# Optimization experiments

Measured on AMD Instinct MI355X. Metric: run time of the kernel, lower is better.

## Reference

```python
import jax, jax.numpy as jnp
import numpy as np

H, HKV, D, W = 64, 8, 64, 128          # heads, kv heads, head_dim, sliding window
G = H // HKV                            # query heads per kv head
HID = 2880
THETA = 150000.0
SCALE = D ** -0.5
NEG = -1e30


def _rope(x, positions):
    # x: [B,S,h,D]; GPT-NeoX style rotate_half RoPE
    half = D // 2
    inv_freq = 1.0 / (THETA ** (jnp.arange(0, half, dtype=jnp.float32) / half))
    ang = positions.astype(jnp.float32)[:, None] * inv_freq          # [S, D/2]
    cos = jnp.cos(ang)[None, :, None, :]
    sin = jnp.sin(ang)[None, :, None, :]
    x1, x2 = x[..., :half], x[..., half:]
    return jnp.concatenate([x1 * cos - x2 * sin, x2 * cos + x1 * sin], axis=-1)


def setup_inputs() -> dict:
    key = jax.random.key(0)
    ks = jax.random.split(key, 6)
    B, S = 1, 2048
    return {
        "hidden_states": jax.random.normal(ks[0], (B, S, HID), jnp.float32),
        "positions": jnp.arange(S, dtype=jnp.int32),
        "w_qkv": jax.random.normal(ks[1], (HID, (H + 2 * HKV) * D), jnp.float32) * 0.02,
        "b_qkv": jax.random.normal(ks[2], ((H + 2 * HKV) * D,), jnp.float32) * 0.02,
        "w_o": jax.random.normal(ks[3], (H * D, HID), jnp.float32) * 0.02,
        "b_o": jax.random.normal(ks[4], (HID,), jnp.float32) * 0.02,
        "sinks": jax.random.normal(ks[5], (H,), jnp.float32),
    }


def reference(hidden_states, positions, w_qkv, b_qkv, w_o, b_o, sinks):
    B, S, _ = hidden_states.shape
    qkv = hidden_states @ w_qkv + b_qkv                               # [B,S,(H+2Hkv)*D]
    q, k, v = jnp.split(qkv, [H * D, H * D + HKV * D], axis=-1)
    Q = q.reshape(B, S, H, D)
    K = k.reshape(B, S, HKV, D)
    V = v.reshape(B, S, HKV, D)
    Q = _rope(Q, positions)
    K = _rope(K, positions)

    # banded (sliding-window) key/value gather: query i sees keys i-W+1..i
    offsets = jnp.arange(W) - (W - 1)                                 # [-(W-1)..0]
    kidx = jnp.arange(S)[:, None] + offsets                           # [S,W]
    valid = kidx >= 0
    kidx = jnp.maximum(kidx, 0)
    Kw = K[:, kidx]                                                    # [B,S,W,HKV,D]
    Vw = V[:, kidx]

    Qr = Q.reshape(B, S, HKV, G, D)                                    # GQA grouping
    scores = jnp.einsum('bskgd,bswkd->bskgw', Qr, Kw) * SCALE          # [B,S,HKV,G,W]
    scores = jnp.where(valid[None, :, None, None, :], scores, NEG)

    sink = sinks.reshape(HKV, G)[None, None]                           # [1,1,HKV,G]
    m = jnp.maximum(scores.max(axis=-1), sink)                         # [B,S,HKV,G]
    p = jnp.exp(scores - m[..., None])
    denom = p.sum(axis=-1) + jnp.exp(sink - m)                         # sink in normalizer
    out = jnp.einsum('bskgw,bswkd->bskgd', p, Vw) / denom[..., None]

    out = out.reshape(B, S, H * D)
    return out @ w_o + b_o
```

## Files before the change

kernel.cpp:

```cpp
#include <hip/hip_runtime.h>

typedef unsigned short u16;
typedef __bf16 bf16x8 __attribute__((ext_vector_type(8)));
typedef float f32x4 __attribute__((ext_vector_type(4)));
typedef unsigned short u16x8 __attribute__((ext_vector_type(8)));

#define QKV_N 5120
#define SEQ 2048
#define ATTN_K 4096
#define KPAD 2944
#define SCALE 0.125f
#define NEGINF -1e30f

__device__ __forceinline__ u16 f2bf(float f) {
  unsigned int u = __builtin_bit_cast(unsigned int, f);
  u = (u + 0x7FFFu + ((u >> 16) & 1u)) >> 16;
  return (u16)u;
}
__device__ __forceinline__ float bf2f(u16 u) {
  unsigned int x = ((unsigned int)u) << 16;
  return __builtin_bit_cast(float, x);
}

#define MFMA16(a, b, c) __builtin_amdgcn_mfma_f32_16x16x32_bf16((a), (b), (c), 0, 0, 0)

__device__ __forceinline__ void gl_lds16(const u16* g, u16* l) {
  __builtin_amdgcn_global_load_lds(
      (const __attribute__((address_space(1))) unsigned int*)(const void*)g,
      (__attribute__((address_space(3))) unsigned int*)(void*)l, 16, 0, 0);
}

__device__ __forceinline__ bf16x8 fragrd(const u16* base, int row, int rb) {
  return *(const bf16x8*)((const char*)(base + row * 32) + rb);
}

__device__ __forceinline__ bf16x8 lds_frag(const u16* mat, int row, int kh, int lg) {
  int off = row * 128 + ((kh * 64 + lg * 16) ^ ((row & 7) << 4));
  return *(const bf16x8*)((const char*)mat + off);
}

__global__ __launch_bounds__(256) void k_rope_table(const int* __restrict__ pos,
                                                    float2* __restrict__ tab) {
  int t = blockIdx.x * 256 + threadIdx.x;
  int s = t >> 5, i = t & 31;
  float freq = powf(150000.0f, -(float)i * (1.0f / 32.0f));
  float ang = (float)pos[s] * freq;
  float sv, cv;
  sincosf(ang, &sv, &cv);
  tab[t] = make_float2(cv, sv);
}

__global__ __launch_bounds__(256) void k_convert_pad(const float* __restrict__ in,
                                                     u16* __restrict__ out) {
  int i = blockIdx.x * 256 + threadIdx.x;
  int r = i / 736, c4 = i - r * 736;
  if (r >= 2048) return;
  ushort4 o = {0, 0, 0, 0};
  if (c4 < 720) {
    float4 v = *(const float4*)(in + (size_t)r * 2880 + c4 * 4);
    o.x = f2bf(v.x); o.y = f2bf(v.y); o.z = f2bf(v.z); o.w = f2bf(v.w);
  }
  ((ushort4*)out)[(size_t)r * 736 + c4] = o;
}

__global__ __launch_bounds__(256) void k_transpose(const float* __restrict__ in,
                                                   u16* __restrict__ out,
                                                   int Kin, int Kout, int Nd, int Npad) {
  __shared__ float tile[32][33];
  int n0 = blockIdx.x * 32, k0 = blockIdx.y * 32;
  int c = threadIdx.x & 31, r0 = threadIdx.x >> 5;
#pragma unroll
  for (int j = 0; j < 4; j++) {
    int r = r0 + j * 8;
    float v = 0.f;
    if (n0 + c < Nd && k0 + r < Kin) v = in[(size_t)(k0 + r) * Nd + n0 + c];
    tile[r][c] = v;
  }
  __syncthreads();
#pragma unroll
  for (int j = 0; j < 4; j++) {
    int rr = r0 + j * 8;
    int n = n0 + rr;
    if (n < Npad) out[(size_t)n * Kout + k0 + c] = f2bf(tile[c][rr]);
  }
}

__global__ __launch_bounds__(256, 2) void k_gemm1(const u16* __restrict__ Ag,
                                                  const u16* __restrict__ Bg,
                                                  const float* __restrict__ bias,
                                                  u16* __restrict__ C) {
  __shared__ u16 lds_[2][18432];
  u16* L = &lds_[0][0];
  const int tid = threadIdx.x;
  const int lane = tid & 63, wave = tid >> 6;
  const int wm = wave >> 1, wn = wave & 1;
  const int lr = lane & 15, lg = lane >> 4;
  const int bid = blockIdx.x;
  const int xcd = bid & 7, j = bid >> 3;
  const int m0 = (j >> 2) * 128;
  const int n0 = (xcd * 4 + (j & 3)) * 160;

  f32x4 acc[4][5] = {};
  bf16x8 Bf[5], Af0, Af1;

  const int rb = (lg * 16) ^ (((lr >> 1) & 3) << 4);
  const int arow = tid >> 2;
  const int axs = ((tid & 3) ^ ((tid >> 3) & 3)) << 3;

  size_t boff[5];
#pragma unroll
  for (int r_ = 0; r_ < 5; r_++) {
    int e = r_ * 2048 + tid * 8;
    int bkh = (e >= 5120) ? 1 : 0;
    int re = e - bkh * 5120;
    int brow = re >> 5;
    int bch = (re >> 3) & 3;
    int bps = bch ^ ((brow >> 1) & 3);
    boff[r_] = (size_t)(n0 + brow) * KPAD + bkh * 32 + bps * 8;
  }

#define STA(b, kh, kt, r_)                                                      \
  gl_lds16(Ag + (size_t)(m0 + (r_) * 64 + arow) * KPAD + (kt) + (kh) * 32 + axs, \
           L + (b) * 18432 + (kh) * 4096 + (r_) * 2048 + wave * 512)
#define STB(b, kt, r_)                                                          \
  gl_lds16(Bg + boff[r_] + (kt), L + (b) * 18432 + 8192 + (r_) * 2048 + wave * 512)
#define RDB(b, kh)                                                              \
  { _Pragma("unroll") for (int nf = 0; nf < 5; nf++)                            \
      Bf[nf] = fragrd(L + (b) * 18432 + 8192 + (kh) * 5120,                     \
                      wn * 80 + nf * 16 + lr, rb); }
#define RDA(b, kh, mf0_)                                                        \
  { Af0 = fragrd(L + (b) * 18432 + (kh) * 4096, wm * 64 + (mf0_) * 16 + lr, rb); \
    Af1 = fragrd(L + (b) * 18432 + (kh) * 4096, wm * 64 + ((mf0_) + 1) * 16 + lr, rb); }
#define MM(ma, mb)                                                              \
  { __builtin_amdgcn_s_setprio(1);                                              \
    _Pragma("unroll") for (int nf = 0; nf < 5; nf++) {                          \
      acc[ma][nf] = MFMA16(Af0, Bf[nf], acc[ma][nf]);                           \
      acc[mb][nf] = MFMA16(Af1, Bf[nf], acc[mb][nf]); }                         \
    __builtin_amdgcn_s_setprio(0); }
#define BAR __builtin_amdgcn_s_barrier();
#define VM4 asm volatile("s_waitcnt vmcnt(4)" ::: "memory");
#define VM0 asm volatile("s_waitcnt vmcnt(0)" ::: "memory");

  STA(0, 0, 0, 0); STA(0, 0, 0, 1);
  STB(0, 0, 0); STB(0, 0, 1); STB(0, 0, 2); STB(0, 0, 3); STB(0, 0, 4);
  STA(0, 1, 0, 0); STA(0, 1, 0, 1);
  VM4 BAR

  for (int t = 0; t < 46; t++) {
    const int b = t & 1, nb = b ^ 1;
    const int kt1 = (t + 1) * 64;
    const bool st = (t < 45);
    RDB(b, 0) RDA(b, 0, 0)
    if (st) { STA(nb, 0, kt1, 0); STA(nb, 0, kt1, 1); STB(nb, kt1, 0); }
    BAR MM(0, 1) BAR
    RDA(b, 0, 2)
    if (st) { STB(nb, kt1, 1); STB(nb, kt1, 2); VM4 } else { VM0 }
    BAR MM(2, 3) BAR
    RDB(b, 1) RDA(b, 1, 0)
    if (st) { STB(nb, kt1, 3); STB(nb, kt1, 4); }
    BAR MM(0, 1) BAR
    RDA(b, 1, 2)
    if (st) { STA(nb, 1, kt1, 0); STA(nb, 1, kt1, 1); VM4 }
    BAR MM(2, 3) BAR
  }
#undef STA
#undef STB
#undef RDB
#undef RDA
#undef MM
#undef BAR
#undef VM4
#undef VM0

#pragma unroll
  for (int mf = 0; mf < 4; mf++)
#pragma unroll
    for (int nf = 0; nf < 5; nf++) {
      int col = n0 + wn * 80 + nf * 16 + lr;
      float bv = bias[col];
#pragma unroll
      for (int rg = 0; rg < 4; rg++) {
        int row = m0 + wm * 64 + mf * 16 + lg * 4 + rg;
        C[(size_t)row * QKV_N + col] = f2bf(acc[mf][nf][rg] + bv);
      }
    }
}

__global__ __launch_bounds__(256, 2) void k_gemm2(const u16* __restrict__ Ag,
                                                  const u16* __restrict__ Bg,
                                                  const float* __restrict__ bias,
                                                  float* __restrict__ C) {
  __shared__ u16 ldsbuf[2][16384];
  const int tid = threadIdx.x;
  const int lane = tid & 63, wave = tid >> 6;
  const int wm = wave >> 1, wn = wave & 1;
  const int lr = lane & 15, lg = lane >> 4;
  int bid = blockIdx.x;
  int l = (bid & 7) * 46 + (bid >> 3);
  const int m0 = (l & 15) * 128, n0 = (l >> 4) * 128;

  f32x4 acc[4][4] = {};

  const int srow = wave * 8 + (lane >> 3);
  const int sc = ((lane & 7) ^ (lane >> 3)) << 3;
  const u16* gA = Ag + (size_t)(m0 + srow) * ATTN_K + sc;
  const u16* gB = Bg + (size_t)(n0 + srow) * ATTN_K + sc;

#define G2_STAGE(kt, b)                                                          \
  {                                                                              \
    u16* Ab = &ldsbuf[b][0];                                                     \
    u16* Bb = &ldsbuf[b][8192];                                                  \
    _Pragma("unroll") for (int r = 0; r < 4; r++) {                              \
      gl_lds16(gA + (size_t)(r * 32) * ATTN_K + (kt), Ab + (r * 32 + wave * 8) * 64); \
      gl_lds16(gB + (size_t)(r * 32) * ATTN_K + (kt), Bb + (r * 32 + wave * 8) * 64); \
    }                                                                            \
  }

  G2_STAGE(0, 0)
  G2_STAGE(64, 1)
  asm volatile("s_waitcnt vmcnt(8)" ::: "memory");
  __builtin_amdgcn_s_barrier();

  for (int t = 0; t < 64; t++) {
    const int b = t & 1;
    const u16* La = &ldsbuf[b][0];
    const u16* Lb = &ldsbuf[b][8192];
    bf16x8 Bf[4][2];
#pragma unroll
    for (int nf = 0; nf < 4; nf++)
#pragma unroll
      for (int kh = 0; kh < 2; kh++)
        Bf[nf][kh] = lds_frag(Lb, wn * 64 + nf * 16 + lr, kh, lg);
    bf16x8 Af[2][2];
#pragma unroll
    for (int mi = 0; mi < 2; mi++)
#pragma unroll
      for (int kh = 0; kh < 2; kh++)
        Af[mi][kh] = lds_frag(La, wm * 64 + mi * 16 + lr, kh, lg);
#pragma unroll
    for (int q = 0; q < 2; q++) {
      bf16x8 An[2][2];
      if (q < 1) {
#pragma unroll
        for (int mi = 0; mi < 2; mi++)
#pragma unroll
          for (int kh = 0; kh < 2; kh++)
            An[mi][kh] = lds_frag(La, wm * 64 + ((q + 1) * 2 + mi) * 16 + lr, kh, lg);
      }
      __builtin_amdgcn_s_setprio(1);
#pragma unroll
      for (int mi = 0; mi < 2; mi++)
#pragma unroll
        for (int nf = 0; nf < 4; nf++)
#pragma unroll
          for (int kh = 0; kh < 2; kh++)
            acc[q * 2 + mi][nf] = MFMA16(Af[mi][kh], Bf[nf][kh], acc[q * 2 + mi][nf]);
      __builtin_amdgcn_s_setprio(0);
      if (q < 1) {
#pragma unroll
        for (int mi = 0; mi < 2; mi++)
#pragma unroll
          for (int kh = 0; kh < 2; kh++)
            Af[mi][kh] = An[mi][kh];
      }
    }
    __builtin_amdgcn_s_barrier();
    if (t <= 61) {
      G2_STAGE((t + 2) * 64, b)
      asm volatile("s_waitcnt vmcnt(8)" ::: "memory");
    } else {
      asm volatile("s_waitcnt vmcnt(0)" ::: "memory");
    }
    __builtin_amdgcn_s_barrier();
  }
#undef G2_STAGE

#pragma unroll
  for (int mi = 0; mi < 4; mi++)
#pragma unroll
    for (int ni = 0; ni < 4; ni++) {
      int row = m0 + wm * 64 + mi * 16 + lg * 4;
      int col = n0 + wn * 64 + ni * 16 + lr;
      if (col < 2880) {
        float bv = bias[col];
#pragma unroll
        for (int rg = 0; rg < 4; rg++)
          C[(size_t)(row + rg) * 2880 + col] = acc[mi][ni][rg] + bv;
      }
    }
}

__global__ __launch_bounds__(512, 2) void k_attn(const u16* __restrict__ qkv,
                                                 const float* __restrict__ sinks,
                                                 const float2* __restrict__ tab,
                                                 u16* __restrict__ out) {
  __shared__ u16 Klds[160 * 64];
  __shared__ u16 Vt[64 * 168];
  __shared__ u16 Pslab[8 * 32 * 40];
  const int hk = blockIdx.y;
  const int s0 = blockIdx.x * 32;
  const int kb = s0 - 127;
  const int tid = threadIdx.x;
  const int lane = tid & 63, w = tid >> 6;
  const int lr = lane & 15, lg = lane >> 4;

  for (int u = tid; u < 160 * 4; u += 512) {
    int key = u >> 2, c = u & 3;
    int kidx = kb + key;
    u16x8 v1 = {0, 0, 0, 0, 0, 0, 0, 0}, v2 = v1;
    if (kidx >= 0 && kidx < SEQ) {
      const u16* base = qkv + (size_t)kidx * QKV_N + 4096 + hk * 64;
      u16x8 x1 = *(const u16x8*)(base + c * 8);
      u16x8 x2 = *(const u16x8*)(base + 32 + c * 8);
      const float2* cs = tab + (size_t)kidx * 32 + c * 8;
#pragma unroll
      for (int j = 0; j < 8; j++) {
        float f1 = bf2f(x1[j]), f2 = bf2f(x2[j]);
        float2 t = cs[j];
        v1[j] = f2bf(f1 * t.x - f2 * t.y);
        v2[j] = f2bf(f2 * t.x + f1 * t.y);
      }
    }
    int o1 = (key * 128 + c * 16) ^ ((key & 7) << 4);
    int o2 = (key * 128 + (c + 4) * 16) ^ ((key & 7) << 4);
    *(u16x8*)((char*)Klds + o1) = v1;
    *(u16x8*)((char*)Klds + o2) = v2;
  }
  for (int e4 = tid; e4 < 160 * 16; e4 += 512) {
    int key = e4 >> 4, d0 = (e4 & 15) * 4;
    int kidx = kb + key;
    ushort4 v = {0, 0, 0, 0};
    if (kidx >= 0 && kidx < SEQ)
      v = *(const ushort4*)(qkv + (size_t)kidx * QKV_N + 4608 + hk * 64 + d0);
    Vt[(d0 + 0) * 168 + key] = v.x;
    Vt[(d0 + 1) * 168 + key] = v.y;
    Vt[(d0 + 2) * 168 + key] = v.z;
    Vt[(d0 + 3) * 168 + key] = v.w;
  }

  const int head = hk * 8 + w;
  bf16x8 qf[2][2];
#pragma unroll
  for (int rt = 0; rt < 2; rt++) {
    int s = s0 + rt * 16 + lr;
    const u16* base = qkv + (size_t)s * QKV_N + head * 64 + lg * 8;
    u16x8 r0 = *(const u16x8*)(base);
    u16x8 r1 = *(const u16x8*)(base + 32);
    const float2* cs = tab + (size_t)s * 32 + lg * 8;
    u16x8 y0, y1;
#pragma unroll
    for (int j = 0; j < 8; j++) {
      float f1 = bf2f(r0[j]), f2 = bf2f(r1[j]);
      float2 t = cs[j];
      y0[j] = f2bf(f1 * t.x - f2 * t.y);
      y1[j] = f2bf(f2 * t.x + f1 * t.y);
    }
    qf[rt][0] = __builtin_bit_cast(bf16x8, y0);
    qf[rt][1] = __builtin_bit_cast(bf16x8, y1);
  }
  __syncthreads();

  f32x4 sc[2][10];
  f32x4 zz = {0.f, 0.f, 0.f, 0.f};
#pragma unroll
  for (int rt = 0; rt < 2; rt++)
#pragma unroll
    for (int nt = 0; nt < 10; nt++) sc[rt][nt] = zz;
#pragma unroll
  for (int nt = 0; nt < 10; nt++) {
    int key = nt * 16 + lr;
#pragma unroll
    for (int ks = 0; ks < 2; ks++) {
      int off = (key * 128 + ks * 64 + lg * 16) ^ ((key & 7) << 4);
      bf16x8 kf = *(const bf16x8*)((const char*)Klds + off);
      sc[0][nt] = MFMA16(qf[0][ks], kf, sc[0][nt]);
      sc[1][nt] = MFMA16(qf[1][ks], kf, sc[1][nt]);
    }
  }

#pragma unroll
  for (int rt = 0; rt < 2; rt++)
#pragma unroll
    for (int nt = 0; nt < 10; nt++)
#pragma unroll
      for (int rg = 0; rg < 4; rg++) {
        int qq = rt * 16 + lg * 4 + rg;
        int j = nt * 16 + lr;
        bool valid = (j >= qq) && (j <= qq + 127) && ((kb + j) >= 0);
        sc[rt][nt][rg] = valid ? sc[rt][nt][rg] * SCALE : NEGINF;
      }

  const float sink = sinks[head];
  float den[2][4];
#pragma unroll
  for (int rt = 0; rt < 2; rt++)
#pragma unroll
    for (int rg = 0; rg < 4; rg++) {
      float m = NEGINF;
#pragma unroll
      for (int nt = 0; nt < 10; nt++) m = fmaxf(m, sc[rt][nt][rg]);
#pragma unroll
      for (int x = 1; x < 16; x <<= 1) m = fmaxf(m, __shfl_xor(m, x, 64));
      m = fmaxf(m, sink);
      float sum = 0.f;
#pragma unroll
      for (int nt = 0; nt < 10; nt++) {
        float p = __expf(sc[rt][nt][rg] - m);
        sc[rt][nt][rg] = p;
        sum += p;
      }
#pragma unroll
      for (int x = 1; x < 16; x <<= 1) sum += __shfl_xor(sum, x, 64);
      den[rt][rg] = sum + __expf(sink - m);
    }

  f32x4 oacc[2][4];
#pragma unroll
  for (int rt = 0; rt < 2; rt++)
#pragma unroll
    for (int dn = 0; dn < 4; dn++) oacc[rt][dn] = zz;
  u16* slab = &Pslab[w * 32 * 40];
#pragma unroll
  for (int kt = 0; kt < 5; kt++) {
#pragma unroll
    for (int rt = 0; rt < 2; rt++)
#pragma unroll
      for (int j2 = 0; j2 < 2; j2++)
#pragma unroll
        for (int rg = 0; rg < 4; rg++)
          slab[(rt * 16 + lg * 4 + rg) * 40 + j2 * 16 + lr] = f2bf(sc[rt][kt * 2 + j2][rg]);
    asm volatile("s_waitcnt lgkmcnt(0)" ::: "memory");
    __builtin_amdgcn_sched_barrier(0);
    bf16x8 pf0 = *(const bf16x8*)&slab[lr * 40 + lg * 8];
    bf16x8 pf1 = *(const bf16x8*)&slab[(16 + lr) * 40 + lg * 8];
#pragma unroll
    for (int dn = 0; dn < 4; dn++) {
      bf16x8 vf = *(const bf16x8*)&Vt[(dn * 16 + lr) * 168 + kt * 32 + lg * 8];
      oacc[0][dn] = MFMA16(pf0, vf, oacc[0][dn]);
      oacc[1][dn] = MFMA16(pf1, vf, oacc[1][dn]);
    }
  }

#pragma unroll
  for (int rt = 0; rt < 2; rt++)
#pragma unroll
    for (int dn = 0; dn < 4; dn++)
#pragma unroll
      for (int rg = 0; rg < 4; rg++) {
        int s = s0 + rt * 16 + lg * 4 + rg;
        float val = oacc[rt][dn][rg] / den[rt][rg];
        out[(size_t)s * ATTN_K + head * 64 + dn * 16 + lr] = f2bf(val);
      }
}

extern "C" void kernel_launch(void* const* d_in, const int* in_sizes, int n_in,
                              void* d_out, int out_size, void* d_ws, size_t ws_size,
                              hipStream_t stream) {
  const float* hs = (const float*)d_in[0];
  const int* pos = (const int*)d_in[1];
  const float* wqkv = (const float*)d_in[2];
  const float* bqkv = (const float*)d_in[3];
  const float* wo = (const float*)d_in[4];
  const float* bo = (const float*)d_in[5];
  const float* sinks = (const float*)d_in[6];
  float* out = (float*)d_out;

  char* ws = (char*)d_ws;
  u16* qkvb = (u16*)(ws + 0);
  u16* hsb = (u16*)(ws + 41943040);
  u16* wqkvT = (u16*)(ws + 54001664);
  u16* attnb = (u16*)(ws + 41943040);
  u16* woT = (u16*)(ws + 84148224);
  float2* tab = (float2*)(ws + 108265472);

  k_rope_table<<<256, 256, 0, stream>>>(pos, tab);
  k_convert_pad<<<5888, 256, 0, stream>>>(hs, hsb);
  k_transpose<<<dim3(160, 92), 256, 0, stream>>>(wqkv, wqkvT, 2880, KPAD, 5120, 5120);
  k_transpose<<<dim3(92, 128), 256, 0, stream>>>(wo, woT, 4096, 4096, 2880, 2944);
  k_gemm1<<<512, 256, 0, stream>>>(hsb, wqkvT, bqkv, qkvb);
  k_attn<<<dim3(64, 8), 512, 0, stream>>>(qkvb, sinks, tab, attnb);
  k_gemm2<<<368, 256, 0, stream>>>(attnb, woT, bo, out);
}
```

Before: 199.1 us.

## Merge gemm1 A-fragment phases and retile gemm2 to 128x96 tiles

In the QKV GEMM, all four A fragments are now loaded at once, so each k-half runs one block of 20 MFMAs instead of two blocks of 10. This halves the barrier pairs per iteration, at the cost of more live registers. The output GEMM switches from 128x128 tiles to 128x96 tiles, which divide 2880 exactly. That removes the wasted padded columns and the bounds check, and it raises the grid from 368 to 480 blocks for better CU balance, at the cost of somewhat lower per-tile reuse.

```diff
diff --git a/kernel.cpp b/kernel.cpp
--- a/kernel.cpp
+++ b/kernel.cpp
@@ -101,7 +101,7 @@
   const int n0 = (xcd * 4 + (j & 3)) * 160;
 
   f32x4 acc[4][5] = {};
-  bf16x8 Bf[5], Af0, Af1;
+  bf16x8 Bf[5], Af0, Af1, Af2, Af3;
 
   const int rb = (lg * 16) ^ (((lr >> 1) & 3) << 4);
   const int arow = tid >> 2;
@@ -128,16 +128,21 @@
   { _Pragma("unroll") for (int nf = 0; nf < 5; nf++)                            \
       Bf[nf] = fragrd(L + (b) * 18432 + 8192 + (kh) * 5120,                     \
                       wn * 80 + nf * 16 + lr, rb); }
-#define RDA(b, kh, mf0_)                                                        \
-  { Af0 = fragrd(L + (b) * 18432 + (kh) * 4096, wm * 64 + (mf0_) * 16 + lr, rb); \
-    Af1 = fragrd(L + (b) * 18432 + (kh) * 4096, wm * 64 + ((mf0_) + 1) * 16 + lr, rb); }
-#define MM(ma, mb)                                                              \
+#define RDA4(b, kh)                                                             \
+  { Af0 = fragrd(L + (b) * 18432 + (kh) * 4096, wm * 64 + 0 * 16 + lr, rb);     \
+    Af1 = fragrd(L + (b) * 18432 + (kh) * 4096, wm * 64 + 1 * 16 + lr, rb);     \
+    Af2 = fragrd(L + (b) * 18432 + (kh) * 4096, wm * 64 + 2 * 16 + lr, rb);     \
+    Af3 = fragrd(L + (b) * 18432 + (kh) * 4096, wm * 64 + 3 * 16 + lr, rb); }
+#define MM20                                                                    \
   { __builtin_amdgcn_s_setprio(1);                                              \
     _Pragma("unroll") for (int nf = 0; nf < 5; nf++) {                          \
-      acc[ma][nf] = MFMA16(Af0, Bf[nf], acc[ma][nf]);                           \
-      acc[mb][nf] = MFMA16(Af1, Bf[nf], acc[mb][nf]); }                         \
+      acc[0][nf] = MFMA16(Af0, Bf[nf], acc[0][nf]);                             \
+      acc[1][nf] = MFMA16(Af1, Bf[nf], acc[1][nf]);                             \
+      acc[2][nf] = MFMA16(Af2, Bf[nf], acc[2][nf]);                             \
+      acc[3][nf] = MFMA16(Af3, Bf[nf], acc[3][nf]); }                           \
     __builtin_amdgcn_s_setprio(0); }
 #define BAR __builtin_amdgcn_s_barrier();
+#define VM5 asm volatile("s_waitcnt vmcnt(5)" ::: "memory");
 #define VM4 asm volatile("s_waitcnt vmcnt(4)" ::: "memory");
 #define VM0 asm volatile("s_waitcnt vmcnt(0)" ::: "memory");
 
@@ -150,25 +155,29 @@
     const int b = t & 1, nb = b ^ 1;
     const int kt1 = (t + 1) * 64;
     const bool st = (t < 45);
-    RDB(b, 0) RDA(b, 0, 0)
-    if (st) { STA(nb, 0, kt1, 0); STA(nb, 0, kt1, 1); STB(nb, kt1, 0); }
-    BAR MM(0, 1) BAR
-    RDA(b, 0, 2)
-    if (st) { STB(nb, kt1, 1); STB(nb, kt1, 2); VM4 } else { VM0 }
-    BAR MM(2, 3) BAR
-    RDB(b, 1) RDA(b, 1, 0)
-    if (st) { STB(nb, kt1, 3); STB(nb, kt1, 4); }
-    BAR MM(0, 1) BAR
-    RDA(b, 1, 2)
-    if (st) { STA(nb, 1, kt1, 0); STA(nb, 1, kt1, 1); VM4 }
-    BAR MM(2, 3) BAR
+    RDB(b, 0) RDA4(b, 0)
+    if (st) {
+      STA(nb, 0, kt1, 0); STA(nb, 0, kt1, 1);
+      STB(nb, kt1, 0); STB(nb, kt1, 1); STB(nb, kt1, 2);
+      VM5
+    } else {
+      VM0
+    }
+    BAR MM20 BAR
+    RDB(b, 1) RDA4(b, 1)
+    if (st) {
+      STB(nb, kt1, 3); STB(nb, kt1, 4);
+      STA(nb, 1, kt1, 0); STA(nb, 1, kt1, 1);
+      VM4
+    }
+    BAR MM20 BAR
   }
 #undef STA
 #undef STB
 #undef RDB
-#undef RDA
-#undef MM
-#undef BAR
+#undef RDA4
+#undef MM20
+#undef VM5
 #undef VM4
 #undef VM0
 
@@ -190,16 +199,16 @@
                                                   const u16* __restrict__ Bg,
                                                   const float* __restrict__ bias,
                                                   float* __restrict__ C) {
-  __shared__ u16 ldsbuf[2][16384];
+  __shared__ u16 ldsbuf[2][14336];
   const int tid = threadIdx.x;
   const int lane = tid & 63, wave = tid >> 6;
   const int wm = wave >> 1, wn = wave & 1;
   const int lr = lane & 15, lg = lane >> 4;
   int bid = blockIdx.x;
-  int l = (bid & 7) * 46 + (bid >> 3);
-  const int m0 = (l & 15) * 128, n0 = (l >> 4) * 128;
-
-  f32x4 acc[4][4] = {};
+  int l = (bid & 7) * 60 + (bid >> 3);
+  const int m0 = (l & 15) * 128, n0 = (l >> 4) * 96;
+
+  f32x4 acc[4][3] = {};
 
   const int srow = wave * 8 + (lane >> 3);
   const int sc = ((lane & 7) ^ (lane >> 3)) << 3;
@@ -210,27 +219,27 @@
   {                                                                              \
     u16* Ab = &ldsbuf[b][0];                                                     \
     u16* Bb = &ldsbuf[b][8192];                                                  \
-    _Pragma("unroll") for (int r = 0; r < 4; r++) {                              \
+    _Pragma("unroll") for (int r = 0; r < 4; r++)                                \
       gl_lds16(gA + (size_t)(r * 32) * ATTN_K + (kt), Ab + (r * 32 + wave * 8) * 64); \
+    _Pragma("unroll") for (int r = 0; r < 3; r++)                                \
       gl_lds16(gB + (size_t)(r * 32) * ATTN_K + (kt), Bb + (r * 32 + wave * 8) * 64); \
-    }                                                                            \
   }
 
   G2_STAGE(0, 0)
   G2_STAGE(64, 1)
-  asm volatile("s_waitcnt vmcnt(8)" ::: "memory");
+  asm volatile("s_waitcnt vmcnt(7)" ::: "memory");
   __builtin_amdgcn_s_barrier();
 
   for (int t = 0; t < 64; t++) {
     const int b = t & 1;
     const u16* La = &ldsbuf[b][0];
     const u16* Lb = &ldsbuf[b][8192];
-    bf16x8 Bf[4][2];
-#pragma unroll
-    for (int nf = 0; nf < 4; nf++)
+    bf16x8 Bf[3][2];
+#pragma unroll
+    for (int nf = 0; nf < 3; nf++)
 #pragma unroll
       for (int kh = 0; kh < 2; kh++)
-        Bf[nf][kh] = lds_frag(Lb, wn * 64 + nf * 16 + lr, kh, lg);
+        Bf[nf][kh] = lds_frag(Lb, wn * 48 + nf * 16 + lr, kh, lg);
     bf16x8 Af[2][2];
 #pragma unroll
     for (int mi = 0; mi < 2; mi++)
@@ -251,7 +260,7 @@
 #pragma unroll
       for (int mi = 0; mi < 2; mi++)
 #pragma unroll
-        for (int nf = 0; nf < 4; nf++)
+        for (int nf = 0; nf < 3; nf++)
 #pragma unroll
           for (int kh = 0; kh < 2; kh++)
             acc[q * 2 + mi][nf] = MFMA16(Af[mi][kh], Bf[nf][kh], acc[q * 2 + mi][nf]);
@@ -267,7 +276,7 @@
     __builtin_amdgcn_s_barrier();
     if (t <= 61) {
       G2_STAGE((t + 2) * 64, b)
-      asm volatile("s_waitcnt vmcnt(8)" ::: "memory");
+      asm volatile("s_waitcnt vmcnt(7)" ::: "memory");
     } else {
       asm volatile("s_waitcnt vmcnt(0)" ::: "memory");
     }
@@ -278,15 +287,13 @@
 #pragma unroll
   for (int mi = 0; mi < 4; mi++)
 #pragma unroll
-    for (int ni = 0; ni < 4; ni++) {
+    for (int ni = 0; ni < 3; ni++) {
       int row = m0 + wm * 64 + mi * 16 + lg * 4;
-      int col = n0 + wn * 64 + ni * 16 + lr;
-      if (col < 2880) {
-        float bv = bias[col];
-#pragma unroll
-        for (int rg = 0; rg < 4; rg++)
-          C[(size_t)(row + rg) * 2880 + col] = acc[mi][ni][rg] + bv;
-      }
+      int col = n0 + wn * 48 + ni * 16 + lr;
+      float bv = bias[col];
+#pragma unroll
+      for (int rg = 0; rg < 4; rg++)
+        C[(size_t)(row + rg) * 2880 + col] = acc[mi][ni][rg] + bv;
     }
 }
 
@@ -479,5 +486,5 @@
   k_transpose<<<dim3(92, 128), 256, 0, stream>>>(wo, woT, 4096, 4096, 2880, 2944);
   k_gemm1<<<512, 256, 0, stream>>>(hsb, wqkvT, bqkv, qkvb);
   k_attn<<<dim3(64, 8), 512, 0, stream>>>(qkvb, sinks, tab, attnb);
-  k_gemm2<<<368, 256, 0, stream>>>(attnb, woT, bo, out);
-}
+  k_gemm2<<<480, 256, 0, stream>>>(attnb, woT, bo, out);
+}
```

Result: faster. 190.8 us (-4.2%).
